# Optimization experiments

Measured on AMD Instinct MI355X. Metric: run time of the kernel, lower is better.

Reference implementation:

```python
import jax, jax.numpy as jnp
import numpy as np

B = 256
DIM_IN = 1024
DIM_GLOBAL = 1024
U = 512          # num_units = sum(num_units_regions)
D = 16           # dim_attention_unit
G = 8            # num_attention_groups
NEG_INF = -jnp.inf


def setup_inputs() -> dict:
    key = jax.random.key(0)
    ks = jax.random.split(key, 8)
    x = jax.random.normal(ks[0], (B, DIM_IN), dtype=jnp.float32)
    # learned params (xavier-ish scale)
    W1 = jax.random.normal(ks[1], (DIM_IN, DIM_GLOBAL), dtype=jnp.float32) * (1.0 / np.sqrt(DIM_IN))
    b1 = jnp.zeros((DIM_GLOBAL,), dtype=jnp.float32)
    W2 = jax.random.normal(ks[2], (DIM_GLOBAL, U * D), dtype=jnp.float32) * (1.0 / np.sqrt(DIM_GLOBAL))
    b2 = jnp.zeros((U * D,), dtype=jnp.float32)
    temperature = jnp.ones((U,), dtype=jnp.float32)
    mem_attention = jax.random.normal(ks[3], (B, U, D), dtype=jnp.float32)
    mem_value = jax.random.normal(ks[4], (B, U, D), dtype=jnp.float32)
    return {"x": x, "W1": W1, "b1": b1, "W2": W2, "b2": b2,
            "temperature": temperature,
            "mem_attention": mem_attention, "mem_value": mem_value}


def reference(x, W1, b1, W2, b2, temperature, mem_attention, mem_value):
    batch = x.shape[0]
    # two-layer linear projection -> per-unit attention keys [B, U, D]
    h = x @ W1 + b1
    attention = (h @ W2 + b2).reshape(batch, U, D)
    # broadcast mul-sum score over d: [B, M, U]  (M == batch)
    weights = jnp.einsum('bud,mud->bmu', attention, mem_attention)
    weights = weights * temperature  # per-unit temperature, broadcasts over last axis
    # mask_p = 0.0 -> random mask is a no-op (per original code's early return)
    # eye mask: query i cannot attend to memory slot i
    eye = jnp.eye(batch, dtype=bool)[:, :, None]
    weights = jnp.where(eye, NEG_INF, weights)
    # grouped softmax over the memory axis within each group of size batch // G
    w = weights.reshape(batch, batch // G, G, U)
    w = jax.nn.softmax(w, axis=1)
    weights = w.reshape(batch, batch, U) / 8.0
    # weighted sum over memory slots: [B, U, D]
    outputs = jnp.einsum('bmu,mud->bud', weights, mem_value)
    return (attention, weights, outputs)
```

## Files before the change

### kernel.cpp

```cpp
#include <hip/hip_runtime.h>
#include <hip/hip_bf16.h>
#include <math.h>

#define Bq 256
#define DIM_IN 1024
#define DIM_GLOBAL 1024
#define UNITS 512
#define DD 16
#define GG 8
#define ATT_ELEMS (256*512*16)
#define W_ELEMS   (256*256*512)
#define SCRATCH_BYTES ((size_t)512*256*256*4)

typedef __attribute__((ext_vector_type(8))) short bf16x8;
typedef __attribute__((ext_vector_type(4))) float f32x4;

__device__ __forceinline__ short f2bf(float f) {
    union { float f; unsigned u; } v; v.f = f;
    unsigned u = v.u;
    u += 0x7fffu + ((u >> 16) & 1u);
    return (short)(u >> 16);
}

__device__ __forceinline__ unsigned pk2(float a, float b) {
    return (unsigned)(unsigned short)f2bf(a) | ((unsigned)(unsigned short)f2bf(b) << 16);
}

#define BK 32
#define ASTR 40
#define BSTR 40

__global__ __launch_bounds__(256) void gemm_bias(
    const float* __restrict__ A, const float* __restrict__ B,
    const float* __restrict__ bias, float* __restrict__ C,
    int M, int N, int K)
{
    __shared__ __align__(16) short As[64 * ASTR];
    __shared__ __align__(16) short Bs[64 * BSTR];

    const int t = threadIdx.x;
    const int lane = t & 63;
    const int wave = t >> 6;
    const int m0 = blockIdx.y * 64;
    const int n0 = blockIdx.x * 64;

    const int wm = (wave >> 1) * 32;
    const int wn = (wave & 1) * 32;
    const int fl = lane & 15;
    const int ko = lane >> 4;

    f32x4 acc00 = {}, acc01 = {}, acc10 = {}, acc11 = {};

    const int ar = t >> 2;
    const int aq = (t & 3) * 8;
    const int bn = t & 63;
    const int bk = (t >> 6) * 8;

    for (int k0 = 0; k0 < K; k0 += BK) {
        __syncthreads();
        {
            const float* src = A + (m0 + ar) * K + k0 + aq;
            float4 v0 = *(const float4*)(src);
            float4 v1 = *(const float4*)(src + 4);
            bf16x8 p;
            p[0]=f2bf(v0.x); p[1]=f2bf(v0.y); p[2]=f2bf(v0.z); p[3]=f2bf(v0.w);
            p[4]=f2bf(v1.x); p[5]=f2bf(v1.y); p[6]=f2bf(v1.z); p[7]=f2bf(v1.w);
            *(bf16x8*)(&As[ar * ASTR + aq]) = p;
        }
        {
            const float* src = B + (k0 + bk) * N + n0 + bn;
            bf16x8 p;
            #pragma unroll
            for (int j = 0; j < 8; j++) p[j] = f2bf(src[j * N]);
            *(bf16x8*)(&Bs[bn * BSTR + bk]) = p;
        }
        __syncthreads();

        bf16x8 a0 = *(const bf16x8*)(&As[(wm + 0  + fl) * ASTR + ko * 8]);
        bf16x8 a1 = *(const bf16x8*)(&As[(wm + 16 + fl) * ASTR + ko * 8]);
        bf16x8 b0 = *(const bf16x8*)(&Bs[(wn + 0  + fl) * BSTR + ko * 8]);
        bf16x8 b1 = *(const bf16x8*)(&Bs[(wn + 16 + fl) * BSTR + ko * 8]);
        acc00 = __builtin_amdgcn_mfma_f32_16x16x32_bf16(a0, b0, acc00, 0, 0, 0);
        acc01 = __builtin_amdgcn_mfma_f32_16x16x32_bf16(a0, b1, acc01, 0, 0, 0);
        acc10 = __builtin_amdgcn_mfma_f32_16x16x32_bf16(a1, b0, acc10, 0, 0, 0);
        acc11 = __builtin_amdgcn_mfma_f32_16x16x32_bf16(a1, b1, acc11, 0, 0, 0);
    }

    #pragma unroll
    for (int r = 0; r < 4; r++) {
        int mrow = m0 + wm + ko * 4 + r;
        int ncol = n0 + wn + fl;
        C[(mrow     ) * N + (ncol     )] = acc00[r] + bias[ncol];
        C[(mrow     ) * N + (ncol + 16)] = acc01[r] + bias[ncol + 16];
        C[(mrow + 16) * N + (ncol     )] = acc10[r] + bias[ncol];
        C[(mrow + 16) * N + (ncol + 16)] = acc11[r] + bias[ncol + 16];
    }
}

#define L2E 1.4426950408889634f

__global__ __launch_bounds__(256) void attn_mfma(
    const float* __restrict__ attention,
    const float* __restrict__ mem_att,
    const float* __restrict__ mem_val,
    const float* __restrict__ temperature,
    float* __restrict__ scratch,
    float* __restrict__ outputs_out)
{
    const int t    = threadIdx.x;
    const int lane = t & 63;
    const int lq   = lane >> 4;
    const int lr   = lane & 15;
    const int bid  = blockIdx.x;
    const int swz  = (bid & 7) * 256 + (bid >> 3);
    const int W    = swz * 4 + (t >> 6);
    const int u    = W >> 4;
    const int bt   = W & 15;
    const bool ldq = (lq < 2);

    const float tl2e = temperature[u] * L2E;
    const f32x4 zf = {0.f, 0.f, 0.f, 0.f};
    const int bg = bt * 16 + lr;

    bf16x8 kf[16];
    #pragma unroll
    for (int mt = 0; mt < 16; mt++) {
        bf16x8 p = {0,0,0,0,0,0,0,0};
        if (ldq) {
            const float* src = mem_att + (size_t)(mt*16 + lr) * 8192 + u * 16 + lq * 8;
            float4 v0 = *(const float4*)(src);
            float4 v1 = *(const float4*)(src + 4);
            p[0]=f2bf(v0.x); p[1]=f2bf(v0.y); p[2]=f2bf(v0.z); p[3]=f2bf(v0.w);
            p[4]=f2bf(v1.x); p[5]=f2bf(v1.y); p[6]=f2bf(v1.z); p[7]=f2bf(v1.w);
        }
        kf[mt] = p;
    }
    bf16x8 af = {0,0,0,0,0,0,0,0};
    if (ldq) {
        const float* src = attention + (size_t)bg * 8192 + u * 16 + lq * 8;
        float4 v0 = *(const float4*)(src);
        float4 v1 = *(const float4*)(src + 4);
        af[0]=f2bf(v0.x); af[1]=f2bf(v0.y); af[2]=f2bf(v0.z); af[3]=f2bf(v0.w);
        af[4]=f2bf(v1.x); af[5]=f2bf(v1.y); af[6]=f2bf(v1.z); af[7]=f2bf(v1.w);
    }

    f32x4 gacc = zf;
    #pragma unroll
    for (int mt = 0; mt < 16; mt++) {
        f32x4 s = __builtin_amdgcn_mfma_f32_16x16x32_bf16(kf[mt], af, zf, 0, 0, 0);
        #pragma unroll
        for (int r = 0; r < 4; r++) {
            const int m = mt*16 + lq*4 + r;
            gacc[r] += (m == bg) ? 0.f : exp2f(s[r] * tl2e);
        }
    }
    f32x4 rinv;
    #pragma unroll
    for (int r = 0; r < 4; r++) {
        const float tot = gacc[r] + __shfl_xor(gacc[r], 32);
        rinv[r] = 1.0f / (8.0f * tot);
    }

    auto load_vpair = [&](int p) -> bf16x8 {
        const float* base = mem_val + (size_t)(p*32 + lq*4) * 8192 + u * 16 + lr;
        bf16x8 vv;
        #pragma unroll
        for (int j = 0; j < 4; j++) {
            vv[j]     = f2bf(base[(size_t)j * 8192]);
            vv[4 + j] = f2bf(base[(size_t)(16 + j) * 8192]);
        }
        return vv;
    };

    f32x4 oacc = zf;
    bf16x8 vf = load_vpair(0);
    float* sbase = scratch + (size_t)u * 65536 + bg;

    #pragma unroll
    for (int p2 = 0; p2 < 8; p2++) {
        const bf16x8 vcur = vf;
        if (p2 < 7) vf = load_vpair(p2 + 1);

        f32x4 sX = __builtin_amdgcn_mfma_f32_16x16x32_bf16(kf[2*p2    ], af, zf, 0, 0, 0);
        f32x4 sY = __builtin_amdgcn_mfma_f32_16x16x32_bf16(kf[2*p2 + 1], af, zf, 0, 0, 0);

        float wX[4], wY[4];
        #pragma unroll
        for (int r = 0; r < 4; r++) {
            const int mX = p2*32 + lq*4 + r;
            const int mY = mX + 16;
            wX[r] = (mX == bg) ? 0.f : exp2f(sX[r] * tl2e) * rinv[r];
            wY[r] = (mY == bg) ? 0.f : exp2f(sY[r] * tl2e) * rinv[r];
        }

        float* spX = sbase + (size_t)(p2*32 + lq*4) * 256;
        #pragma unroll
        for (int r = 0; r < 4; r++) spX[(size_t)r * 256] = wX[r];
        float* spY = spX + 16 * 256;
        #pragma unroll
        for (int r = 0; r < 4; r++) spY[(size_t)r * 256] = wY[r];

        union { unsigned uu[4]; bf16x8 v; } wf;
        wf.uu[0] = pk2(wX[0], wX[1]);
        wf.uu[1] = pk2(wX[2], wX[3]);
        wf.uu[2] = pk2(wY[0], wY[1]);
        wf.uu[3] = pk2(wY[2], wY[3]);
        oacc = __builtin_amdgcn_mfma_f32_16x16x32_bf16(wf.v, vcur, oacc, 0, 0, 0);
    }

    #pragma unroll
    for (int r = 0; r < 4; r++) {
        const int bo = bt*16 + lq*4 + r;
        outputs_out[(size_t)bo * 8192 + u * 16 + lr] = oacc[r];
    }
}

__global__ __launch_bounds__(256) void w_transpose(
    const float* __restrict__ scr, float* __restrict__ wout)
{
    const int t    = threadIdx.x;
    const int lane = t & 63;
    const int bx   = blockIdx.x;
    const int m    = bx & 255;
    const int u0   = ((bx >> 8) & 7) << 6;
    const int bt16 = (bx >> 11) * 4 + (t >> 6);
    const int U    = u0 + 4 * (lane & 15);
    const int B    = bt16 * 16 + 4 * (lane >> 4);

    float4 ld[4];
    #pragma unroll
    for (int i = 0; i < 4; i++)
        ld[i] = *(const float4*)(scr + ((size_t)(U + i) << 16) + (m << 8) + B);
    #pragma unroll
    for (int j = 0; j < 4; j++) {
        float4 v;
        v.x = ld[0][j]; v.y = ld[1][j]; v.z = ld[2][j]; v.w = ld[3][j];
        *(float4*)(wout + ((size_t)(B + j) << 17) + (m << 9) + U) = v;
    }
}

__global__ __launch_bounds__(256) void attn_fused_fb(
    const float* __restrict__ attention,
    const float* __restrict__ mem_att,
    const float* __restrict__ mem_val,
    const float* __restrict__ temperature,
    float* __restrict__ weights_out,
    float* __restrict__ outputs_out)
{
    const int t = threadIdx.x;
    const int ublk = blockIdx.x & 15;
    const int bblk = blockIdx.x >> 4;
    const int u  = ublk * 32 + (t & 31);
    const int b  = bblk * 8 + (t >> 5);

    float att[16];
    {
        const float* ap = attention + (size_t)(b * UNITS + u) * DD;
        #pragma unroll
        for (int d4 = 0; d4 < 4; d4++) {
            float4 v = *(const float4*)(ap + d4 * 4);
            att[d4*4+0]=v.x; att[d4*4+1]=v.y; att[d4*4+2]=v.z; att[d4*4+3]=v.w;
        }
    }
    const float tl2e = temperature[u] * L2E;
    const float* kbase = mem_att + u * DD;

    float gsum[8];
    #pragma unroll
    for (int g = 0; g < 8; g++) gsum[g] = 0.f;

    for (int m8 = 0; m8 < 256; m8 += 8) {
        #pragma unroll
        for (int g = 0; g < 8; g++) {
            const int m = m8 + g;
            const float* kp = kbase + m * (UNITS * DD);
            float s = 0.f;
            #pragma unroll
            for (int d4 = 0; d4 < 4; d4++) {
                float4 v = *(const float4*)(kp + d4 * 4);
                s += att[d4*4+0]*v.x + att[d4*4+1]*v.y
                   + att[d4*4+2]*v.z + att[d4*4+3]*v.w;
            }
            const float e = (m == b) ? 0.f : exp2f(s * tl2e);
            gsum[g] += e;
        }
    }
    float rinv[8];
    #pragma unroll
    for (int g = 0; g < 8; g++) rinv[g] = 1.0f / (8.0f * gsum[g]);

    float acc[16];
    #pragma unroll
    for (int d = 0; d < 16; d++) acc[d] = 0.f;
    const float* vbase = mem_val + u * DD;
    float* wrow = weights_out + (size_t)b * (256 * UNITS) + u;

    for (int m8 = 0; m8 < 256; m8 += 8) {
        #pragma unroll
        for (int g = 0; g < 8; g++) {
            const int m = m8 + g;
            const float* kp = kbase + m * (UNITS * DD);
            float s = 0.f;
            #pragma unroll
            for (int d4 = 0; d4 < 4; d4++) {
                float4 v = *(const float4*)(kp + d4 * 4);
                s += att[d4*4+0]*v.x + att[d4*4+1]*v.y
                   + att[d4*4+2]*v.z + att[d4*4+3]*v.w;
            }
            const float e = (m == b) ? 0.f : exp2f(s * tl2e);
            const float w = e * rinv[g];
            wrow[(size_t)m * UNITS] = w;
            const float* vp = vbase + m * (UNITS * DD);
            #pragma unroll
            for (int d4 = 0; d4 < 4; d4++) {
                float4 v = *(const float4*)(vp + d4 * 4);
                acc[d4*4+0] += w * v.x; acc[d4*4+1] += w * v.y;
                acc[d4*4+2] += w * v.z; acc[d4*4+3] += w * v.w;
            }
        }
    }
    float* op = outputs_out + (size_t)(b * UNITS + u) * DD;
    #pragma unroll
    for (int d4 = 0; d4 < 4; d4++) {
        float4 v;
        v.x = acc[d4*4+0]; v.y = acc[d4*4+1];
        v.z = acc[d4*4+2]; v.w = acc[d4*4+3];
        *(float4*)(op + d4 * 4) = v;
    }
}

extern "C" void kernel_launch(void* const* d_in, const int* in_sizes, int n_in,
                              void* d_out, int out_size, void* d_ws, size_t ws_size,
                              hipStream_t stream) {
    const float* x        = (const float*)d_in[0];
    const float* W1       = (const float*)d_in[1];
    const float* b1       = (const float*)d_in[2];
    const float* W2       = (const float*)d_in[3];
    const float* b2       = (const float*)d_in[4];
    const float* temp     = (const float*)d_in[5];
    const float* mem_att  = (const float*)d_in[6];
    const float* mem_val  = (const float*)d_in[7];

    float* out       = (float*)d_out;
    float* attention = out;
    float* weights   = out + ATT_ELEMS;
    float* outputs   = out + ATT_ELEMS + W_ELEMS;

    float* h = weights;

    dim3 blk(256);
    gemm_bias<<<dim3(DIM_GLOBAL / 64, Bq / 64), blk, 0, stream>>>(
        x, W1, b1, h, Bq, DIM_GLOBAL, DIM_IN);
    gemm_bias<<<dim3((UNITS * DD) / 64, Bq / 64), blk, 0, stream>>>(
        h, W2, b2, attention, Bq, UNITS * DD, DIM_GLOBAL);

    if (ws_size >= SCRATCH_BYTES && d_ws != nullptr) {
        float* scratch = (float*)d_ws;
        attn_mfma<<<dim3(2048), blk, 0, stream>>>(
            attention, mem_att, mem_val, temp, scratch, outputs);
        w_transpose<<<dim3(8192), blk, 0, stream>>>(scratch, weights);
    } else {
        attn_fused_fb<<<dim3(512), blk, 0, stream>>>(
            attention, mem_att, mem_val, temp, weights, outputs);
    }
}
```

Before: 362.1 us.

## Fuse weight transpose into attention kernel via LDS, split-K first GEMM

The attention kernel now processes 8 units per 512-thread block. It stages each 32-row slab of softmax weights in double-buffered LDS and writes them straight to the final [B,M,U] layout with vector stores. This removes the 256 MB scratch round trip and the separate transpose kernel. Separately, the first GEMM is split four ways along K with atomic accumulation into a zeroed buffer, and the second GEMM uses a BK=64 tile so there are fewer barriers per MFMA. The costs are a barrier every iteration in the attention loop, atomic traffic, and an extra zeroing launch.

Measured after the change: 415.4 us. 1.15x slower.

```diff
diff --git a/kernel.cpp b/kernel.cpp
--- a/kernel.cpp
+++ b/kernel.cpp
@@ -10,7 +10,6 @@
 #define GG 8
 #define ATT_ELEMS (256*512*16)
 #define W_ELEMS   (256*256*512)
-#define SCRATCH_BYTES ((size_t)512*256*256*4)
 
 typedef __attribute__((ext_vector_type(8))) short bf16x8;
 typedef __attribute__((ext_vector_type(4))) float f32x4;
@@ -26,23 +25,27 @@
     return (unsigned)(unsigned short)f2bf(a) | ((unsigned)(unsigned short)f2bf(b) << 16);
 }
 
+__global__ __launch_bounds__(256) void zero_h(float4* p) {
+    p[blockIdx.x * 256 + threadIdx.x] = make_float4(0.f, 0.f, 0.f, 0.f);
+}
+
 #define BK 32
 #define ASTR 40
-#define BSTR 40
-
-__global__ __launch_bounds__(256) void gemm_bias(
+
+__global__ __launch_bounds__(256) void gemm1_splitk(
     const float* __restrict__ A, const float* __restrict__ B,
     const float* __restrict__ bias, float* __restrict__ C,
     int M, int N, int K)
 {
     __shared__ __align__(16) short As[64 * ASTR];
-    __shared__ __align__(16) short Bs[64 * BSTR];
+    __shared__ __align__(16) short Bs[64 * ASTR];
 
     const int t = threadIdx.x;
     const int lane = t & 63;
     const int wave = t >> 6;
     const int m0 = blockIdx.y * 64;
     const int n0 = blockIdx.x * 64;
+    const int kq = blockIdx.z;
 
     const int wm = (wave >> 1) * 32;
     const int wn = (wave & 1) * 32;
@@ -56,10 +59,11 @@
     const int bn = t & 63;
     const int bk = (t >> 6) * 8;
 
-    for (int k0 = 0; k0 < K; k0 += BK) {
+    const int kbeg = kq * 256;
+    for (int k0 = kbeg; k0 < kbeg + 256; k0 += BK) {
         __syncthreads();
         {
-            const float* src = A + (m0 + ar) * K + k0 + aq;
+            const float* src = A + (size_t)(m0 + ar) * K + k0 + aq;
             float4 v0 = *(const float4*)(src);
             float4 v1 = *(const float4*)(src + 4);
             bf16x8 p;
@@ -68,54 +72,139 @@
             *(bf16x8*)(&As[ar * ASTR + aq]) = p;
         }
         {
-            const float* src = B + (k0 + bk) * N + n0 + bn;
+            const float* src = B + (size_t)(k0 + bk) * N + n0 + bn;
             bf16x8 p;
             #pragma unroll
-            for (int j = 0; j < 8; j++) p[j] = f2bf(src[j * N]);
-            *(bf16x8*)(&Bs[bn * BSTR + bk]) = p;
+            for (int j = 0; j < 8; j++) p[j] = f2bf(src[(size_t)j * N]);
+            *(bf16x8*)(&Bs[bn * ASTR + bk]) = p;
         }
         __syncthreads();
 
         bf16x8 a0 = *(const bf16x8*)(&As[(wm + 0  + fl) * ASTR + ko * 8]);
         bf16x8 a1 = *(const bf16x8*)(&As[(wm + 16 + fl) * ASTR + ko * 8]);
-        bf16x8 b0 = *(const bf16x8*)(&Bs[(wn + 0  + fl) * BSTR + ko * 8]);
-        bf16x8 b1 = *(const bf16x8*)(&Bs[(wn + 16 + fl) * BSTR + ko * 8]);
+        bf16x8 b0 = *(const bf16x8*)(&Bs[(wn + 0  + fl) * ASTR + ko * 8]);
+        bf16x8 b1 = *(const bf16x8*)(&Bs[(wn + 16 + fl) * ASTR + ko * 8]);
         acc00 = __builtin_amdgcn_mfma_f32_16x16x32_bf16(a0, b0, acc00, 0, 0, 0);
         acc01 = __builtin_amdgcn_mfma_f32_16x16x32_bf16(a0, b1, acc01, 0, 0, 0);
         acc10 = __builtin_amdgcn_mfma_f32_16x16x32_bf16(a1, b0, acc10, 0, 0, 0);
         acc11 = __builtin_amdgcn_mfma_f32_16x16x32_bf16(a1, b1, acc11, 0, 0, 0);
     }
 
+    const float bz = (kq == 0) ? 1.f : 0.f;
     #pragma unroll
     for (int r = 0; r < 4; r++) {
         int mrow = m0 + wm + ko * 4 + r;
         int ncol = n0 + wn + fl;
-        C[(mrow     ) * N + (ncol     )] = acc00[r] + bias[ncol];
-        C[(mrow     ) * N + (ncol + 16)] = acc01[r] + bias[ncol + 16];
-        C[(mrow + 16) * N + (ncol     )] = acc10[r] + bias[ncol];
-        C[(mrow + 16) * N + (ncol + 16)] = acc11[r] + bias[ncol + 16];
+        atomicAdd(&C[(size_t)(mrow     ) * N + (ncol     )], acc00[r] + bz * bias[ncol]);
+        atomicAdd(&C[(size_t)(mrow     ) * N + (ncol + 16)], acc01[r] + bz * bias[ncol + 16]);
+        atomicAdd(&C[(size_t)(mrow + 16) * N + (ncol     )], acc10[r] + bz * bias[ncol]);
+        atomicAdd(&C[(size_t)(mrow + 16) * N + (ncol + 16)], acc11[r] + bz * bias[ncol + 16]);
+    }
+}
+
+#define STR2 72
+
+__global__ __launch_bounds__(256) void gemm_bias_bk64(
+    const float* __restrict__ A, const float* __restrict__ B,
+    const float* __restrict__ bias, float* __restrict__ C,
+    int M, int N, int K)
+{
+    __shared__ __align__(16) short As[64 * STR2];
+    __shared__ __align__(16) short Bs[64 * STR2];
+
+    const int t = threadIdx.x;
+    const int lane = t & 63;
+    const int wave = t >> 6;
+    const int m0 = blockIdx.y * 64;
+    const int n0 = blockIdx.x * 64;
+
+    const int wm = (wave >> 1) * 32;
+    const int wn = (wave & 1) * 32;
+    const int fl = lane & 15;
+    const int ko = lane >> 4;
+
+    f32x4 acc00 = {}, acc01 = {}, acc10 = {}, acc11 = {};
+
+    const int ar = t >> 3;
+    const int aq = (t & 7) * 8;
+    const int bn = t & 63;
+    const int bk = (t >> 6) * 8;
+
+    for (int k0 = 0; k0 < K; k0 += 64) {
+        __syncthreads();
+        #pragma unroll
+        for (int h = 0; h < 2; h++) {
+            const float* src = A + (size_t)(m0 + ar + h*32) * K + k0 + aq;
+            float4 v0 = *(const float4*)(src);
+            float4 v1 = *(const float4*)(src + 4);
+            bf16x8 p;
+            p[0]=f2bf(v0.x); p[1]=f2bf(v0.y); p[2]=f2bf(v0.z); p[3]=f2bf(v0.w);
+            p[4]=f2bf(v1.x); p[5]=f2bf(v1.y); p[6]=f2bf(v1.z); p[7]=f2bf(v1.w);
+            *(bf16x8*)(&As[(ar + h*32) * STR2 + aq]) = p;
+        }
+        #pragma unroll
+        for (int h = 0; h < 2; h++) {
+            const float* src = B + (size_t)(k0 + bk + h*32) * N + n0 + bn;
+            bf16x8 p;
+            #pragma unroll
+            for (int j = 0; j < 8; j++) p[j] = f2bf(src[(size_t)j * N]);
+            *(bf16x8*)(&Bs[bn * STR2 + bk + h*32]) = p;
+        }
+        __syncthreads();
+
+        bf16x8 a00 = *(const bf16x8*)(&As[(wm + 0  + fl) * STR2 + ko * 8]);
+        bf16x8 a01 = *(const bf16x8*)(&As[(wm + 0  + fl) * STR2 + ko * 8 + 32]);
+        bf16x8 a10 = *(const bf16x8*)(&As[(wm + 16 + fl) * STR2 + ko * 8]);
+        bf16x8 a11 = *(const bf16x8*)(&As[(wm + 16 + fl) * STR2 + ko * 8 + 32]);
+        bf16x8 b00 = *(const bf16x8*)(&Bs[(wn + 0  + fl) * STR2 + ko * 8]);
+        bf16x8 b01 = *(const bf16x8*)(&Bs[(wn + 0  + fl) * STR2 + ko * 8 + 32]);
+        bf16x8 b10 = *(const bf16x8*)(&Bs[(wn + 16 + fl) * STR2 + ko * 8]);
+        bf16x8 b11 = *(const bf16x8*)(&Bs[(wn + 16 + fl) * STR2 + ko * 8 + 32]);
+        acc00 = __builtin_amdgcn_mfma_f32_16x16x32_bf16(a00, b00, acc00, 0, 0, 0);
+        acc00 = __builtin_amdgcn_mfma_f32_16x16x32_bf16(a01, b01, acc00, 0, 0, 0);
+        acc01 = __builtin_amdgcn_mfma_f32_16x16x32_bf16(a00, b10, acc01, 0, 0, 0);
+        acc01 = __builtin_amdgcn_mfma_f32_16x16x32_bf16(a01, b11, acc01, 0, 0, 0);
+        acc10 = __builtin_amdgcn_mfma_f32_16x16x32_bf16(a10, b00, acc10, 0, 0, 0);
+        acc10 = __builtin_amdgcn_mfma_f32_16x16x32_bf16(a11, b01, acc10, 0, 0, 0);
+        acc11 = __builtin_amdgcn_mfma_f32_16x16x32_bf16(a10, b10, acc11, 0, 0, 0);
+        acc11 = __builtin_amdgcn_mfma_f32_16x16x32_bf16(a11, b11, acc11, 0, 0, 0);
+    }
+
+    #pragma unroll
+    for (int r = 0; r < 4; r++) {
+        int mrow = m0 + wm + ko * 4 + r;
+        int ncol = n0 + wn + fl;
+        C[(size_t)(mrow     ) * N + (ncol     )] = acc00[r] + bias[ncol];
+        C[(size_t)(mrow     ) * N + (ncol + 16)] = acc01[r] + bias[ncol + 16];
+        C[(size_t)(mrow + 16) * N + (ncol     )] = acc10[r] + bias[ncol];
+        C[(size_t)(mrow + 16) * N + (ncol + 16)] = acc11[r] + bias[ncol + 16];
     }
 }
 
 #define L2E 1.4426950408889634f
-
-__global__ __launch_bounds__(256) void attn_mfma(
+#define UPAD 9
+
+__global__ __launch_bounds__(512) void attn_mfma_fused(
     const float* __restrict__ attention,
     const float* __restrict__ mem_att,
     const float* __restrict__ mem_val,
     const float* __restrict__ temperature,
-    float* __restrict__ scratch,
+    float* __restrict__ weights_out,
     float* __restrict__ outputs_out)
 {
+    __shared__ float wlds[2][32 * 16 * UPAD];
+
     const int t    = threadIdx.x;
     const int lane = t & 63;
     const int lq   = lane >> 4;
     const int lr   = lane & 15;
+    const int wv   = t >> 6;
     const int bid  = blockIdx.x;
-    const int swz  = (bid & 7) * 256 + (bid >> 3);
-    const int W    = swz * 4 + (t >> 6);
-    const int u    = W >> 4;
-    const int bt   = W & 15;
+    const int sw   = (bid & 7) * 128 + (bid >> 3);
+    const int ug   = sw >> 4;
+    const int bt   = sw & 15;
+    const int u0   = ug * 8;
+    const int u    = u0 + wv;
     const bool ldq = (lq < 2);
 
     const float tl2e = temperature[u] * L2E;
@@ -174,9 +263,12 @@
 
     f32x4 oacc = zf;
     bf16x8 vf = load_vpair(0);
-    float* sbase = scratch + (size_t)u * 65536 + bg;
-
-    #pragma unroll
+
+    const int m5 = t >> 4;
+    const int b4 = t & 15;
+    float* gflush = weights_out + (size_t)(bt*16 + b4) * 131072 + (size_t)m5 * 512 + u0;
+
+    #pragma unroll 1
     for (int p2 = 0; p2 < 8; p2++) {
         const bf16x8 vcur = vf;
         if (p2 < 7) vf = load_vpair(p2 + 1);
@@ -193,12 +285,12 @@
             wY[r] = (mY == bg) ? 0.f : exp2f(sY[r] * tl2e) * rinv[r];
         }
 
-        float* spX = sbase + (size_t)(p2*32 + lq*4) * 256;
-        #pragma unroll
-        for (int r = 0; r < 4; r++) spX[(size_t)r * 256] = wX[r];
-        float* spY = spX + 16 * 256;
-        #pragma unroll
-        for (int r = 0; r < 4; r++) spY[(size_t)r * 256] = wY[r];
+        float* Lb = wlds[p2 & 1];
+        #pragma unroll
+        for (int r = 0; r < 4; r++) {
+            Lb[((lq*4 + r)      * 16 + lr) * UPAD + wv] = wX[r];
+            Lb[((16 + lq*4 + r) * 16 + lr) * UPAD + wv] = wY[r];
+        }
 
         union { unsigned uu[4]; bf16x8 v; } wf;
         wf.uu[0] = pk2(wX[0], wX[1]);
@@ -206,126 +298,24 @@
         wf.uu[2] = pk2(wY[0], wY[1]);
         wf.uu[3] = pk2(wY[2], wY[3]);
         oacc = __builtin_amdgcn_mfma_f32_16x16x32_bf16(wf.v, vcur, oacc, 0, 0, 0);
+
+        __syncthreads();
+
+        {
+            const float* Ls = &wlds[p2 & 1][(m5 * 16 + b4) * UPAD];
+            float4 lo, hi;
+            lo.x = Ls[0]; lo.y = Ls[1]; lo.z = Ls[2]; lo.w = Ls[3];
+            hi.x = Ls[4]; hi.y = Ls[5]; hi.z = Ls[6]; hi.w = Ls[7];
+            float* gp = gflush + (size_t)(p2 * 32) * 512;
+            *(float4*)(gp)     = lo;
+            *(float4*)(gp + 4) = hi;
+        }
     }
 
     #pragma unroll
     for (int r = 0; r < 4; r++) {
         const int bo = bt*16 + lq*4 + r;
         outputs_out[(size_t)bo * 8192 + u * 16 + lr] = oacc[r];
-    }
-}
-
-__global__ __launch_bounds__(256) void w_transpose(
-    const float* __restrict__ scr, float* __restrict__ wout)
-{
-    const int t    = threadIdx.x;
-    const int lane = t & 63;
-    const int bx   = blockIdx.x;
-    const int m    = bx & 255;
-    const int u0   = ((bx >> 8) & 7) << 6;
-    const int bt16 = (bx >> 11) * 4 + (t >> 6);
-    const int U    = u0 + 4 * (lane & 15);
-    const int B    = bt16 * 16 + 4 * (lane >> 4);
-
-    float4 ld[4];
-    #pragma unroll
-    for (int i = 0; i < 4; i++)
-        ld[i] = *(const float4*)(scr + ((size_t)(U + i) << 16) + (m << 8) + B);
-    #pragma unroll
-    for (int j = 0; j < 4; j++) {
-        float4 v;
-        v.x = ld[0][j]; v.y = ld[1][j]; v.z = ld[2][j]; v.w = ld[3][j];
-        *(float4*)(wout + ((size_t)(B + j) << 17) + (m << 9) + U) = v;
-    }
-}
-
-__global__ __launch_bounds__(256) void attn_fused_fb(
-    const float* __restrict__ attention,
-    const float* __restrict__ mem_att,
-    const float* __restrict__ mem_val,
-    const float* __restrict__ temperature,
-    float* __restrict__ weights_out,
-    float* __restrict__ outputs_out)
-{
-    const int t = threadIdx.x;
-    const int ublk = blockIdx.x & 15;
-    const int bblk = blockIdx.x >> 4;
-    const int u  = ublk * 32 + (t & 31);
-    const int b  = bblk * 8 + (t >> 5);
-
-    float att[16];
-    {
-        const float* ap = attention + (size_t)(b * UNITS + u) * DD;
-        #pragma unroll
-        for (int d4 = 0; d4 < 4; d4++) {
-            float4 v = *(const float4*)(ap + d4 * 4);
-            att[d4*4+0]=v.x; att[d4*4+1]=v.y; att[d4*4+2]=v.z; att[d4*4+3]=v.w;
-        }
-    }
-    const float tl2e = temperature[u] * L2E;
-    const float* kbase = mem_att + u * DD;
-
-    float gsum[8];
-    #pragma unroll
-    for (int g = 0; g < 8; g++) gsum[g] = 0.f;
-
-    for (int m8 = 0; m8 < 256; m8 += 8) {
-        #pragma unroll
-        for (int g = 0; g < 8; g++) {
-            const int m = m8 + g;
-            const float* kp = kbase + m * (UNITS * DD);
-            float s = 0.f;
-            #pragma unroll
-            for (int d4 = 0; d4 < 4; d4++) {
-                float4 v = *(const float4*)(kp + d4 * 4);
-                s += att[d4*4+0]*v.x + att[d4*4+1]*v.y
-                   + att[d4*4+2]*v.z + att[d4*4+3]*v.w;
-            }
-            const float e = (m == b) ? 0.f : exp2f(s * tl2e);
-            gsum[g] += e;
-        }
-    }
-    float rinv[8];
-    #pragma unroll
-    for (int g = 0; g < 8; g++) rinv[g] = 1.0f / (8.0f * gsum[g]);
-
-    float acc[16];
-    #pragma unroll
-    for (int d = 0; d < 16; d++) acc[d] = 0.f;
-    const float* vbase = mem_val + u * DD;
-    float* wrow = weights_out + (size_t)b * (256 * UNITS) + u;
-
-    for (int m8 = 0; m8 < 256; m8 += 8) {
-        #pragma unroll
-        for (int g = 0; g < 8; g++) {
-            const int m = m8 + g;
-            const float* kp = kbase + m * (UNITS * DD);
-            float s = 0.f;
-            #pragma unroll
-            for (int d4 = 0; d4 < 4; d4++) {
-                float4 v = *(const float4*)(kp + d4 * 4);
-                s += att[d4*4+0]*v.x + att[d4*4+1]*v.y
-                   + att[d4*4+2]*v.z + att[d4*4+3]*v.w;
-            }
-            const float e = (m == b) ? 0.f : exp2f(s * tl2e);
-            const float w = e * rinv[g];
-            wrow[(size_t)m * UNITS] = w;
-            const float* vp = vbase + m * (UNITS * DD);
-            #pragma unroll
-            for (int d4 = 0; d4 < 4; d4++) {
-                float4 v = *(const float4*)(vp + d4 * 4);
-                acc[d4*4+0] += w * v.x; acc[d4*4+1] += w * v.y;
-                acc[d4*4+2] += w * v.z; acc[d4*4+3] += w * v.w;
-            }
-        }
-    }
-    float* op = outputs_out + (size_t)(b * UNITS + u) * DD;
-    #pragma unroll
-    for (int d4 = 0; d4 < 4; d4++) {
-        float4 v;
-        v.x = acc[d4*4+0]; v.y = acc[d4*4+1];
-        v.z = acc[d4*4+2]; v.w = acc[d4*4+3];
-        *(float4*)(op + d4 * 4) = v;
     }
 }
 
@@ -349,18 +339,11 @@
     float* h = weights;
 
     dim3 blk(256);
-    gemm_bias<<<dim3(DIM_GLOBAL / 64, Bq / 64), blk, 0, stream>>>(
+    zero_h<<<dim3(256), blk, 0, stream>>>((float4*)h);
+    gemm1_splitk<<<dim3(DIM_GLOBAL / 64, Bq / 64, 4), blk, 0, stream>>>(
         x, W1, b1, h, Bq, DIM_GLOBAL, DIM_IN);
-    gemm_bias<<<dim3((UNITS * DD) / 64, Bq / 64), blk, 0, stream>>>(
+    gemm_bias_bk64<<<dim3((UNITS * DD) / 64, Bq / 64), blk, 0, stream>>>(
         h, W2, b2, attention, Bq, UNITS * DD, DIM_GLOBAL);
-
-    if (ws_size >= SCRATCH_BYTES && d_ws != nullptr) {
-        float* scratch = (float*)d_ws;
-        attn_mfma<<<dim3(2048), blk, 0, stream>>>(
-            attention, mem_att, mem_val, temp, scratch, outputs);
-        w_transpose<<<dim3(8192), blk, 0, stream>>>(scratch, weights);
-    } else {
-        attn_fused_fb<<<dim3(512), blk, 0, stream>>>(
-            attention, mem_att, mem_val, temp, weights, outputs);
-    }
-}
+    attn_mfma_fused<<<dim3(1024), dim3(512), 0, stream>>>(
+        attention, mem_att, mem_val, temp, weights, outputs);
+}
```
